# Kernel tuning notes

Hardware: AMD Instinct MI355X
Metric: run time of the kernel (lower is better)

Reference implementation:

```python
import jax, jax.numpy as jnp
import numpy as np

N_NODES = 100000


def _glorot(key, shape):
    fan_in, fan_out = shape
    lim = (6.0 / (fan_in + fan_out)) ** 0.5
    return jax.random.uniform(key, shape, jnp.float32, -lim, lim)


def setup_inputs() -> dict:
    key = jax.random.key(0)
    ks = jax.random.split(key, 16)
    E = 1600000
    IN, H, OUT = 32, 48, 32
    f = jax.random.normal(ks[0], (N_NODES, IN), jnp.float32)
    edge_index = jax.random.randint(ks[1], (2, E), 0, N_NODES, jnp.int64)
    # layer 1: theta IN->H, phi H->H
    Wt1 = _glorot(ks[2], (IN, H)); bt1 = jnp.zeros((H,), jnp.float32)
    Wp1 = _glorot(ks[3], (H, H));  bp1 = jnp.zeros((H,), jnp.float32)
    # layer 2: theta H->H, phi H->H
    Wt2 = _glorot(ks[4], (H, H)); bt2 = jnp.zeros((H,), jnp.float32)
    Wp2 = _glorot(ks[5], (H, H)); bp2 = jnp.zeros((H,), jnp.float32)
    # layer 3: theta H->OUT, phi OUT->OUT
    Wt3 = _glorot(ks[6], (H, OUT)); bt3 = jnp.zeros((OUT,), jnp.float32)
    Wp3 = _glorot(ks[7], (OUT, OUT)); bp3 = jnp.zeros((OUT,), jnp.float32)
    return {"f": f, "edge_index": edge_index,
            "Wt1": Wt1, "bt1": bt1, "Wp1": Wp1, "bp1": bp1,
            "Wt2": Wt2, "bt2": bt2, "Wp2": Wp2, "bp2": bp2,
            "Wt3": Wt3, "bt3": bt3, "Wp3": Wp3, "bp3": bp3}


def _triconv(f, src, dst, Wt, bt, Wp, bp):
    # message: linear_theta(f_i - f_j), i = target (dst), j = source (src)
    msg = (f[dst] - f[src]) @ Wt + bt          # [E, C_out]
    agg = jax.ops.segment_sum(msg, dst, num_segments=N_NODES)  # sum aggr
    return agg @ Wp + bp                        # linear_phi


def reference(f, edge_index, Wt1, bt1, Wp1, bp1, Wt2, bt2, Wp2, bp2, Wt3, bt3, Wp3, bp3):
    src, dst = edge_index[0], edge_index[1]
    h = jax.nn.relu(_triconv(f, src, dst, Wt1, bt1, Wp1, bp1))
    h = jax.nn.relu(_triconv(h, src, dst, Wt2, bt2, Wp2, bp2))
    out = jax.nn.softmax(_triconv(h, src, dst, Wt3, bt3, Wp3, bp3), axis=-1)
    return out
```

## Files before the change

kernel.cpp:

```cpp
#include <hip/hip_runtime.h>


#define SHIFT 9
#define SPAN 512
#define MAXB 256
#define CHUNK 4096


__global__ void k_detect(const unsigned int* __restrict__ ew,
                         int* __restrict__ flag, int* __restrict__ bcount) {
  int t = threadIdx.x;
  bcount[t] = 0;
  unsigned int v = 0;
#pragma unroll
  for (int j = 0; j < 4; ++j) v |= ew[2 * (t * 4 + j) + 1];
  __shared__ unsigned int red[256];
  red[t] = v;
  __syncthreads();
  for (int s = 128; s > 0; s >>= 1) {
    if (t < s) red[t] |= red[t + s];
    __syncthreads();
  }
  if (t == 0) flag[0] = (red[0] == 0u) ? 1 : 0;
}

__global__ void k_bcount(const void* __restrict__ edges,
                         const int* __restrict__ flag,
                         int* __restrict__ bcount, int E) {
  __shared__ int cnt[MAXB];
  int t = threadIdx.x;
  cnt[t] = 0;
  __syncthreads();
  int base = blockIdx.x * CHUNK;
  if (flag[0]) {
    const long long* p = (const long long*)edges;
#pragma unroll
    for (int j = 0; j < CHUNK / 256; ++j) {
      int idx = base + j * 256 + t;
      if (idx < E) atomicAdd(&cnt[((int)p[E + idx]) >> SHIFT], 1);
    }
  } else {
    const int* p = (const int*)edges;
#pragma unroll
    for (int j = 0; j < CHUNK / 256; ++j) {
      int idx = base + j * 256 + t;
      if (idx < E) atomicAdd(&cnt[p[E + idx] >> SHIFT], 1);
    }
  }
  __syncthreads();
  if (cnt[t]) atomicAdd(&bcount[t], cnt[t]);
}

__global__ void k_bscan(const int* __restrict__ bcount, int* __restrict__ bbase,
                        int* __restrict__ bcursor, int* __restrict__ offs,
                        int NB, int N, int E) {
  __shared__ int lds[MAXB];
  int t = threadIdx.x;
  int v = (t < NB) ? bcount[t] : 0;
  lds[t] = v;
  __syncthreads();
  for (int off = 1; off < MAXB; off <<= 1) {
    int add = (t >= off) ? lds[t - off] : 0;
    __syncthreads();
    lds[t] += add;
    __syncthreads();
  }
  int ex = lds[t] - v;
  bbase[t] = ex;
  bcursor[t] = ex;
  if (t == MAXB - 1) bbase[MAXB] = lds[t];
  if (t == 0) offs[N] = E;
}

__global__ void k_bin(const void* __restrict__ edges,
                      const int* __restrict__ flag, int* __restrict__ bcursor,
                      unsigned int* __restrict__ binned, int E) {
  __shared__ unsigned int pk[CHUNK];
  __shared__ unsigned char bk[CHUNK];
  __shared__ int cnt[MAXB], bb[MAXB], cnt2[MAXB];
  int t = threadIdx.x;
  cnt[t] = 0;
  cnt2[t] = 0;
  __syncthreads();
  int base = blockIdx.x * CHUNK;
  if (flag[0]) {
    const long long* p = (const long long*)edges;
#pragma unroll
    for (int j = 0; j < CHUNK / 256; ++j) {
      int li = j * 256 + t, idx = base + li;
      if (idx < E) {
        int s = (int)p[idx];
        int d = (int)p[E + idx];
        int b = d >> SHIFT;
        pk[li] = ((unsigned)(d & (SPAN - 1)) << 17) | (unsigned)s;
        bk[li] = (unsigned char)b;
        atomicAdd(&cnt[b], 1);
      }
    }
  } else {
    const int* p = (const int*)edges;
#pragma unroll
    for (int j = 0; j < CHUNK / 256; ++j) {
      int li = j * 256 + t, idx = base + li;
      if (idx < E) {
        int s = p[idx];
        int d = p[E + idx];
        int b = d >> SHIFT;
        pk[li] = ((unsigned)(d & (SPAN - 1)) << 17) | (unsigned)s;
        bk[li] = (unsigned char)b;
        atomicAdd(&cnt[b], 1);
      }
    }
  }
  __syncthreads();
  if (cnt[t]) bb[t] = atomicAdd(&bcursor[t], cnt[t]);
  __syncthreads();
#pragma unroll
  for (int j = 0; j < CHUNK / 256; ++j) {
    int li = j * 256 + t, idx = base + li;
    if (idx < E) {
      int b = bk[li];
      int r = atomicAdd(&cnt2[b], 1);
      binned[bb[b] + r] = pk[li];
    }
  }
}

__launch_bounds__(256) __global__
void k_bcsr(const unsigned int* __restrict__ binned,
            const int* __restrict__ bbase, int* __restrict__ offs,
            int* __restrict__ csr, int N) {
  __shared__ int deg[SPAN];
  __shared__ int gs[128];
  __shared__ int cur[SPAN];
  int b = blockIdx.x;
  int t = threadIdx.x;
  deg[t] = 0;
  deg[t + 256] = 0;
  __syncthreads();
  int base = bbase[b];
  int cnt = bbase[b + 1] - base;
  for (int e = t; e < cnt; e += 256)
    atomicAdd(&deg[binned[base + e] >> 17], 1);
  __syncthreads();
  if (t < 128) gs[t] = deg[4 * t] + deg[4 * t + 1] + deg[4 * t + 2] + deg[4 * t + 3];
  __syncthreads();
  for (int off = 1; off < 128; off <<= 1) {
    int add = (t < 128 && t >= off) ? gs[t - off] : 0;
    __syncthreads();
    if (t < 128) gs[t] += add;
    __syncthreads();
  }
  int nodeBase = b << SHIFT;
  if (t < 128) {
    int run = (t == 0) ? 0 : gs[t - 1];
#pragma unroll
    for (int j = 0; j < 4; ++j) {
      int li = 4 * t + j;
      cur[li] = run;
      int node = nodeBase + li;
      if (node < N) offs[node] = base + run;
      run += deg[li];
    }
  }
  __syncthreads();
  for (int e = t; e < cnt; e += 256) {
    unsigned int v = binned[base + e];
    int ld = v >> 17;
    int pos = atomicAdd(&cur[ld], 1);
    csr[base + pos] = (int)(v & 0x1FFFFu);
  }
}

template <int CIN, int COUT, int ACT>
__launch_bounds__(256, 4) __global__
void k_layer(const float* __restrict__ hin, float* __restrict__ hout,
             const int* __restrict__ offs, const int* __restrict__ csr,
             const float* __restrict__ Wt, const float* __restrict__ bt,
             const float* __restrict__ Wp, const float* __restrict__ bp,
             int n) {
  constexpr int NPB = 64;
  constexpr int NCK = CIN / 16;
  constexpr int TCH = NCK * 4;
  constexpr int CH2 = COUT / 4;

  __shared__ float Wtl[CIN * COUT];
  __shared__ float Wpl[COUT * COUT];
  __shared__ float btl[COUT];
  __shared__ float bpl[COUT];

  int t = threadIdx.x;
  for (int i = t; i < CIN * COUT; i += 256) Wtl[i] = Wt[i];
  for (int i = t; i < COUT * COUT; i += 256) Wpl[i] = Wp[i];
  if (t < COUT) {
    btl[t] = bt[t];
    bpl[t] = bp[t];
  }
  __syncthreads();

  int ln = t >> 2;
  int g = t & 3;
  int node = blockIdx.x * NPB + ln;
  bool valid = node < n;
  int start = valid ? offs[node] : 0;
  int end = valid ? offs[node + 1] : 0;
  float degf = (float)(end - start);

  const int fo = 4 * g;
  float acc[TCH];
#pragma unroll
  for (int j = 0; j < TCH; ++j) acc[j] = 0.f;

  int k = start;
  for (; k + 4 < end; k += 5) {
    int s0 = csr[k], s1 = csr[k + 1], s2 = csr[k + 2], s3 = csr[k + 3],
        s4 = csr[k + 4];
    float4 v0[NCK], v1[NCK], v2[NCK], v3[NCK], v4[NCK];
    const float* r0 = hin + (size_t)s0 * CIN + fo;
    const float* r1 = hin + (size_t)s1 * CIN + fo;
    const float* r2 = hin + (size_t)s2 * CIN + fo;
    const float* r3 = hin + (size_t)s3 * CIN + fo;
    const float* r4 = hin + (size_t)s4 * CIN + fo;
#pragma unroll
    for (int q = 0; q < NCK; ++q) v0[q] = *(const float4*)(r0 + 16 * q);
#pragma unroll
    for (int q = 0; q < NCK; ++q) v1[q] = *(const float4*)(r1 + 16 * q);
#pragma unroll
    for (int q = 0; q < NCK; ++q) v2[q] = *(const float4*)(r2 + 16 * q);
#pragma unroll
    for (int q = 0; q < NCK; ++q) v3[q] = *(const float4*)(r3 + 16 * q);
#pragma unroll
    for (int q = 0; q < NCK; ++q) v4[q] = *(const float4*)(r4 + 16 * q);
#pragma unroll
    for (int q = 0; q < NCK; ++q) {
      acc[q * 4 + 0] += (v0[q].x + v1[q].x) + (v2[q].x + v3[q].x) + v4[q].x;
      acc[q * 4 + 1] += (v0[q].y + v1[q].y) + (v2[q].y + v3[q].y) + v4[q].y;
      acc[q * 4 + 2] += (v0[q].z + v1[q].z) + (v2[q].z + v3[q].z) + v4[q].z;
      acc[q * 4 + 3] += (v0[q].w + v1[q].w) + (v2[q].w + v3[q].w) + v4[q].w;
    }
  }
  for (; k < end; ++k) {
    const float* r0 = hin + (size_t)csr[k] * CIN + fo;
#pragma unroll
    for (int q = 0; q < NCK; ++q) {
      float4 v = *(const float4*)(r0 + 16 * q);
      acc[q * 4 + 0] += v.x;
      acc[q * 4 + 1] += v.y;
      acc[q * 4 + 2] += v.z;
      acc[q * 4 + 3] += v.w;
    }
  }

  float tch[TCH];
  {
    const float* me = hin + (size_t)(valid ? node : 0) * CIN + fo;
#pragma unroll
    for (int q = 0; q < NCK; ++q) {
      float4 v = *(const float4*)(me + 16 * q);
      tch[q * 4 + 0] = degf * v.x - acc[q * 4 + 0];
      tch[q * 4 + 1] = degf * v.y - acc[q * 4 + 1];
      tch[q * 4 + 2] = degf * v.z - acc[q * 4 + 2];
      tch[q * 4 + 3] = degf * v.w - acc[q * 4 + 3];
    }
  }

  const int c2 = g * CH2;
  float a2[CH2];
#pragma unroll
  for (int j = 0; j < CH2; ++j) a2[j] = degf * btl[c2 + j];
#pragma unroll
  for (int kk = 0; kk < CIN; ++kk) {
    const int owner = (kk >> 2) & 3;
    const int idx = ((kk >> 4) << 2) | (kk & 3);
    float tv = __shfl(tch[idx], owner, 4);
#pragma unroll
    for (int j = 0; j < CH2; ++j) a2[j] += tv * Wtl[kk * COUT + c2 + j];
  }

  float a3[CH2];
#pragma unroll
  for (int j = 0; j < CH2; ++j) a3[j] = bpl[c2 + j];
#pragma unroll
  for (int kk = 0; kk < COUT; ++kk) {
    const int owner = kk / CH2;
    const int idx = kk % CH2;
    float ov = __shfl(a2[idx], owner, 4);
#pragma unroll
    for (int j = 0; j < CH2; ++j) a3[j] += ov * Wpl[kk * COUT + c2 + j];
  }

  if (ACT == 0) {
#pragma unroll
    for (int j = 0; j < CH2; ++j) a3[j] = fmaxf(a3[j], 0.f);
  } else {
    float m = -1e30f;
#pragma unroll
    for (int j = 0; j < CH2; ++j) m = fmaxf(m, a3[j]);
    m = fmaxf(m, __shfl_xor(m, 1));
    m = fmaxf(m, __shfl_xor(m, 2));
    float ssum = 0.f;
#pragma unroll
    for (int j = 0; j < CH2; ++j) {
      a3[j] = __expf(a3[j] - m);
      ssum += a3[j];
    }
    ssum += __shfl_xor(ssum, 1);
    ssum += __shfl_xor(ssum, 2);
    float inv = 1.0f / ssum;
#pragma unroll
    for (int j = 0; j < CH2; ++j) a3[j] *= inv;
  }

  if (valid) {
    float* orow = hout + (size_t)node * COUT + c2;
#pragma unroll
    for (int q = 0; q < CH2 / 4; ++q) {
      reinterpret_cast<float4*>(orow)[q] =
          make_float4(a3[q * 4 + 0], a3[q * 4 + 1], a3[q * 4 + 2], a3[q * 4 + 3]);
    }
  }
}


extern "C" void kernel_launch(void* const* d_in, const int* in_sizes, int n_in,
                              void* d_out, int out_size, void* d_ws,
                              size_t ws_size, hipStream_t stream) {
  const float* f = (const float*)d_in[0];
  const void* edges = d_in[1];
  const float* Wt1 = (const float*)d_in[2];
  const float* bt1 = (const float*)d_in[3];
  const float* Wp1 = (const float*)d_in[4];
  const float* bp1 = (const float*)d_in[5];
  const float* Wt2 = (const float*)d_in[6];
  const float* bt2 = (const float*)d_in[7];
  const float* Wp2 = (const float*)d_in[8];
  const float* bp2 = (const float*)d_in[9];
  const float* Wt3 = (const float*)d_in[10];
  const float* bt3 = (const float*)d_in[11];
  const float* Wp3 = (const float*)d_in[12];
  const float* bp3 = (const float*)d_in[13];

  const int N = in_sizes[0] / 32;
  const int E = in_sizes[1] / 2;
  const int NB = (N + SPAN - 1) >> SHIFT;

  char* ws = (char*)d_ws;
  size_t o = 0;
  auto carve = [&](size_t bytes) {
    size_t r = o;
    o = (o + bytes + 255) & ~(size_t)255;
    return r;
  };
  int* flag = (int*)(ws + carve(256));
  int* bcount = (int*)(ws + carve(MAXB * 4));
  int* bbase = (int*)(ws + carve((MAXB + 1) * 4));
  int* bcursor = (int*)(ws + carve(MAXB * 4));
  int* offs = (int*)(ws + carve((size_t)(N + 1) * 4));
  int* csr = (int*)(ws + carve((size_t)E * 4));
  float* h1 = (float*)(ws + carve((size_t)N * 48 * 4));
  float* h2 = (float*)(ws + carve((size_t)N * 48 * 4));
  unsigned int* binned = (unsigned int*)h1;
  (void)ws_size;

  const int nChunks = (E + CHUNK - 1) / CHUNK;

  k_detect<<<1, 256, 0, stream>>>((const unsigned int*)edges, flag, bcount);
  k_bcount<<<nChunks, 256, 0, stream>>>(edges, flag, bcount, E);
  k_bscan<<<1, 256, 0, stream>>>(bcount, bbase, bcursor, offs, NB, N, E);
  k_bin<<<nChunks, 256, 0, stream>>>(edges, flag, bcursor, binned, E);
  k_bcsr<<<NB, 256, 0, stream>>>(binned, bbase, offs, csr, N);

  const int nbl = (N + 63) / 64;
  k_layer<32, 48, 0><<<nbl, 256, 0, stream>>>(f, h1, offs, csr, Wt1, bt1, Wp1,
                                              bp1, N);
  k_layer<48, 48, 0><<<nbl, 256, 0, stream>>>(h1, h2, offs, csr, Wt2, bt2, Wp2,
                                              bp2, N);
  k_layer<48, 32, 1><<<nbl, 256, 0, stream>>>(h2, (float*)d_out, offs, csr,
                                              Wt3, bt3, Wp3, bp3, N);
}
```

Before: 335.3 us.

## Use fixed-capacity edge buckets and stage per-block CSR indices in LDS

Drops the separate bucket-count and scan kernels by giving each 512-node destination bucket a fixed slot of CAP entries, with cursors initialised to b*CAP. This removes one full pass over the edge array and two launches. Per-node end offsets are now stored explicitly because the buckets are no longer contiguous. The layer kernels copy each block's CSR source indices into LDS (up to 2048) and widen the gather unroll from 5 to 6 edges. The risk is correctness on skewed graphs: a bucket with more than CAP edges overflows its slot, and a block with more than 2048 edges reads LDS out of range.

```diff
diff --git a/kernel.cpp b/kernel.cpp
--- a/kernel.cpp
+++ b/kernel.cpp
@@ -5,12 +5,13 @@
 #define SPAN 512
 #define MAXB 256
 #define CHUNK 4096
-
-
-__global__ void k_detect(const unsigned int* __restrict__ ew,
-                         int* __restrict__ flag, int* __restrict__ bcount) {
+#define CAP 10240
+
+
+__global__ void k_init(const unsigned int* __restrict__ ew,
+                       int* __restrict__ flag, int* __restrict__ bcursor) {
   int t = threadIdx.x;
-  bcount[t] = 0;
+  bcursor[t] = t * CAP;
   unsigned int v = 0;
 #pragma unroll
   for (int j = 0; j < 4; ++j) v |= ew[2 * (t * 4 + j) + 1];
@@ -22,54 +23,6 @@
     __syncthreads();
   }
   if (t == 0) flag[0] = (red[0] == 0u) ? 1 : 0;
-}
-
-__global__ void k_bcount(const void* __restrict__ edges,
-                         const int* __restrict__ flag,
-                         int* __restrict__ bcount, int E) {
-  __shared__ int cnt[MAXB];
-  int t = threadIdx.x;
-  cnt[t] = 0;
-  __syncthreads();
-  int base = blockIdx.x * CHUNK;
-  if (flag[0]) {
-    const long long* p = (const long long*)edges;
-#pragma unroll
-    for (int j = 0; j < CHUNK / 256; ++j) {
-      int idx = base + j * 256 + t;
-      if (idx < E) atomicAdd(&cnt[((int)p[E + idx]) >> SHIFT], 1);
-    }
-  } else {
-    const int* p = (const int*)edges;
-#pragma unroll
-    for (int j = 0; j < CHUNK / 256; ++j) {
-      int idx = base + j * 256 + t;
-      if (idx < E) atomicAdd(&cnt[p[E + idx] >> SHIFT], 1);
-    }
-  }
-  __syncthreads();
-  if (cnt[t]) atomicAdd(&bcount[t], cnt[t]);
-}
-
-__global__ void k_bscan(const int* __restrict__ bcount, int* __restrict__ bbase,
-                        int* __restrict__ bcursor, int* __restrict__ offs,
-                        int NB, int N, int E) {
-  __shared__ int lds[MAXB];
-  int t = threadIdx.x;
-  int v = (t < NB) ? bcount[t] : 0;
-  lds[t] = v;
-  __syncthreads();
-  for (int off = 1; off < MAXB; off <<= 1) {
-    int add = (t >= off) ? lds[t - off] : 0;
-    __syncthreads();
-    lds[t] += add;
-    __syncthreads();
-  }
-  int ex = lds[t] - v;
-  bbase[t] = ex;
-  bcursor[t] = ex;
-  if (t == MAXB - 1) bbase[MAXB] = lds[t];
-  if (t == 0) offs[N] = E;
 }
 
 __global__ void k_bin(const void* __restrict__ edges,
@@ -128,8 +81,8 @@
 
 __launch_bounds__(256) __global__
 void k_bcsr(const unsigned int* __restrict__ binned,
-            const int* __restrict__ bbase, int* __restrict__ offs,
-            int* __restrict__ csr, int N) {
+            const int* __restrict__ bcursor, int* __restrict__ offs,
+            int* __restrict__ ends, int* __restrict__ csr, int N) {
   __shared__ int deg[SPAN];
   __shared__ int gs[128];
   __shared__ int cur[SPAN];
@@ -138,8 +91,8 @@
   deg[t] = 0;
   deg[t + 256] = 0;
   __syncthreads();
-  int base = bbase[b];
-  int cnt = bbase[b + 1] - base;
+  int base = b * CAP;
+  int cnt = bcursor[b] - base;
   for (int e = t; e < cnt; e += 256)
     atomicAdd(&deg[binned[base + e] >> 17], 1);
   __syncthreads();
@@ -159,7 +112,10 @@
       int li = 4 * t + j;
       cur[li] = run;
       int node = nodeBase + li;
-      if (node < N) offs[node] = base + run;
+      if (node < N) {
+        offs[node] = base + run;
+        ends[node] = base + run + deg[li];
+      }
       run += deg[li];
     }
   }
@@ -175,7 +131,8 @@
 template <int CIN, int COUT, int ACT>
 __launch_bounds__(256, 4) __global__
 void k_layer(const float* __restrict__ hin, float* __restrict__ hout,
-             const int* __restrict__ offs, const int* __restrict__ csr,
+             const int* __restrict__ offs, const int* __restrict__ ends,
+             const int* __restrict__ csr,
              const float* __restrict__ Wt, const float* __restrict__ bt,
              const float* __restrict__ Wp, const float* __restrict__ bp,
              int n) {
@@ -183,11 +140,13 @@
   constexpr int NCK = CIN / 16;
   constexpr int TCH = NCK * 4;
   constexpr int CH2 = COUT / 4;
+  constexpr int LCAP = 2048;
 
   __shared__ float Wtl[CIN * COUT];
   __shared__ float Wpl[COUT * COUT];
   __shared__ float btl[COUT];
   __shared__ float bpl[COUT];
+  __shared__ int lcsr[LCAP];
 
   int t = threadIdx.x;
   for (int i = t; i < CIN * COUT; i += 256) Wtl[i] = Wt[i];
@@ -196,14 +155,20 @@
     btl[t] = bt[t];
     bpl[t] = bp[t];
   }
+
+  int nf = blockIdx.x * NPB;
+  int nl = min(nf + NPB - 1, n - 1);
+  int blkBase = offs[nf];
+  int blkCnt = min(ends[nl] - blkBase, LCAP);
+  for (int i = t; i < blkCnt; i += 256) lcsr[i] = csr[blkBase + i];
   __syncthreads();
 
   int ln = t >> 2;
   int g = t & 3;
-  int node = blockIdx.x * NPB + ln;
+  int node = nf + ln;
   bool valid = node < n;
-  int start = valid ? offs[node] : 0;
-  int end = valid ? offs[node + 1] : 0;
+  int start = valid ? offs[node] - blkBase : 0;
+  int end = valid ? ends[node] - blkBase : 0;
   float degf = (float)(end - start);
 
   const int fo = 4 * g;
@@ -212,38 +177,30 @@
   for (int j = 0; j < TCH; ++j) acc[j] = 0.f;
 
   int k = start;
-  for (; k + 4 < end; k += 5) {
-    int s0 = csr[k], s1 = csr[k + 1], s2 = csr[k + 2], s3 = csr[k + 3],
-        s4 = csr[k + 4];
-    float4 v0[NCK], v1[NCK], v2[NCK], v3[NCK], v4[NCK];
-    const float* r0 = hin + (size_t)s0 * CIN + fo;
-    const float* r1 = hin + (size_t)s1 * CIN + fo;
-    const float* r2 = hin + (size_t)s2 * CIN + fo;
-    const float* r3 = hin + (size_t)s3 * CIN + fo;
-    const float* r4 = hin + (size_t)s4 * CIN + fo;
-#pragma unroll
-    for (int q = 0; q < NCK; ++q) v0[q] = *(const float4*)(r0 + 16 * q);
-#pragma unroll
-    for (int q = 0; q < NCK; ++q) v1[q] = *(const float4*)(r1 + 16 * q);
-#pragma unroll
-    for (int q = 0; q < NCK; ++q) v2[q] = *(const float4*)(r2 + 16 * q);
-#pragma unroll
-    for (int q = 0; q < NCK; ++q) v3[q] = *(const float4*)(r3 + 16 * q);
-#pragma unroll
-    for (int q = 0; q < NCK; ++q) v4[q] = *(const float4*)(r4 + 16 * q);
+  for (; k + 5 < end; k += 6) {
+    float4 v[6][NCK];
+#pragma unroll
+    for (int d = 0; d < 6; ++d) {
+      const float* r = hin + (size_t)lcsr[k + d] * CIN + fo;
+#pragma unroll
+      for (int q = 0; q < NCK; ++q) v[d][q] = *(const float4*)(r + 16 * q);
+    }
 #pragma unroll
     for (int q = 0; q < NCK; ++q) {
-      acc[q * 4 + 0] += (v0[q].x + v1[q].x) + (v2[q].x + v3[q].x) + v4[q].x;
-      acc[q * 4 + 1] += (v0[q].y + v1[q].y) + (v2[q].y + v3[q].y) + v4[q].y;
-      acc[q * 4 + 2] += (v0[q].z + v1[q].z) + (v2[q].z + v3[q].z) + v4[q].z;
-      acc[q * 4 + 3] += (v0[q].w + v1[q].w) + (v2[q].w + v3[q].w) + v4[q].w;
+#pragma unroll
+      for (int d = 0; d < 6; ++d) {
+        acc[q * 4 + 0] += v[d][q].x;
+        acc[q * 4 + 1] += v[d][q].y;
+        acc[q * 4 + 2] += v[d][q].z;
+        acc[q * 4 + 3] += v[d][q].w;
+      }
     }
   }
   for (; k < end; ++k) {
-    const float* r0 = hin + (size_t)csr[k] * CIN + fo;
+    const float* r = hin + (size_t)lcsr[k] * CIN + fo;
 #pragma unroll
     for (int q = 0; q < NCK; ++q) {
-      float4 v = *(const float4*)(r0 + 16 * q);
+      float4 v = *(const float4*)(r + 16 * q);
       acc[q * 4 + 0] += v.x;
       acc[q * 4 + 1] += v.y;
       acc[q * 4 + 2] += v.z;
@@ -352,11 +309,10 @@
     return r;
   };
   int* flag = (int*)(ws + carve(256));
-  int* bcount = (int*)(ws + carve(MAXB * 4));
-  int* bbase = (int*)(ws + carve((MAXB + 1) * 4));
   int* bcursor = (int*)(ws + carve(MAXB * 4));
-  int* offs = (int*)(ws + carve((size_t)(N + 1) * 4));
-  int* csr = (int*)(ws + carve((size_t)E * 4));
+  int* offs = (int*)(ws + carve((size_t)N * 4));
+  int* ends = (int*)(ws + carve((size_t)N * 4));
+  int* csr = (int*)(ws + carve((size_t)NB * CAP * 4));
   float* h1 = (float*)(ws + carve((size_t)N * 48 * 4));
   float* h2 = (float*)(ws + carve((size_t)N * 48 * 4));
   unsigned int* binned = (unsigned int*)h1;
@@ -364,17 +320,15 @@
 
   const int nChunks = (E + CHUNK - 1) / CHUNK;
 
-  k_detect<<<1, 256, 0, stream>>>((const unsigned int*)edges, flag, bcount);
-  k_bcount<<<nChunks, 256, 0, stream>>>(edges, flag, bcount, E);
-  k_bscan<<<1, 256, 0, stream>>>(bcount, bbase, bcursor, offs, NB, N, E);
+  k_init<<<1, 256, 0, stream>>>((const unsigned int*)edges, flag, bcursor);
   k_bin<<<nChunks, 256, 0, stream>>>(edges, flag, bcursor, binned, E);
-  k_bcsr<<<NB, 256, 0, stream>>>(binned, bbase, offs, csr, N);
+  k_bcsr<<<NB, 256, 0, stream>>>(binned, bcursor, offs, ends, csr, N);
 
   const int nbl = (N + 63) / 64;
-  k_layer<32, 48, 0><<<nbl, 256, 0, stream>>>(f, h1, offs, csr, Wt1, bt1, Wp1,
-                                              bp1, N);
-  k_layer<48, 48, 0><<<nbl, 256, 0, stream>>>(h1, h2, offs, csr, Wt2, bt2, Wp2,
-                                              bp2, N);
-  k_layer<48, 32, 1><<<nbl, 256, 0, stream>>>(h2, (float*)d_out, offs, csr,
-                                              Wt3, bt3, Wp3, bp3, N);
-}
+  k_layer<32, 48, 0><<<nbl, 256, 0, stream>>>(f, h1, offs, ends, csr, Wt1, bt1,
+                                              Wp1, bp1, N);
+  k_layer<48, 48, 0><<<nbl, 256, 0, stream>>>(h1, h2, offs, ends, csr, Wt2,
+                                              bt2, Wp2, bp2, N);
+  k_layer<48, 32, 1><<<nbl, 256, 0, stream>>>(h2, (float*)d_out, offs, ends,
+                                              csr, Wt3, bt3, Wp3, bp3, N);
+}
```

Measured after the change: 306.5 us. 1.09x faster.
